# Kernel optimization log

Measured on AMD Instinct MI355X. Metric: run time of the kernel, lower is better.

Reference implementation:

```python
import jax, jax.numpy as jnp
import numpy as np

B = 2048          # number of graphs in the batch
ACT_DIM = 14      # nodes per graph (act_dim)
C = 128           # in_channels
H = 256           # hidden_size


def _pair_edges(n):
    ii, jj = np.meshgrid(np.arange(n), np.arange(n), indexing='ij')
    m = ii != jj
    return np.stack([ii[m], jj[m]], axis=1)  # [n*(n-1), 2]


def setup_inputs() -> dict:
    key = jax.random.key(0)
    ks = jax.random.split(key, 12)
    edges_np = _pair_edges(ACT_DIM)                       # [182, 2]
    offs = (np.arange(B) * ACT_DIM)[:, None, None]
    batched = (edges_np[None] + offs).reshape(-1, 2)      # [B*182, 2]
    edge_index = jnp.asarray(batched.T, dtype=jnp.int64 if jax.config.jax_enable_x64 else jnp.int32)
    edges = jnp.asarray(edges_np, dtype=jnp.int32)

    def lin(k, o, i):
        return jax.random.normal(k, (o, i), jnp.float32) * (1.0 / np.sqrt(i))

    return {
        'state': jax.random.normal(ks[0], (B * ACT_DIM, C), jnp.float32),
        'conv_w': lin(ks[1], C, C),
        'conv_b': jnp.zeros((C,), jnp.float32),
        'lin1_w': lin(ks[2], H, 2 * C),
        'lin1_b': jax.random.normal(ks[3], (H,), jnp.float32) * 0.01,
        'lin2_w': lin(ks[4], H, H),
        'lin2_b': jax.random.normal(ks[5], (H,), jnp.float32) * 0.01,
        'mu_w': lin(ks[6], 1, H),
        'mu_b': jnp.zeros((1,), jnp.float32),
        'sig_w': lin(ks[7], 1, H),
        'sig_b': jnp.zeros((1,), jnp.float32),
        'noise': jax.random.normal(ks[8], (B, edges_np.shape[0]), jnp.float32),
        'edge_index': edge_index,
        'edges': edges,
    }


def _gcn_conv(x, edge_index, w, b):
    # Standard GCNConv: add self-loops, symmetric normalization, x @ W^T, scatter-add, + bias.
    n = x.shape[0]
    loops = jnp.arange(n, dtype=edge_index.dtype)
    src = jnp.concatenate([edge_index[0], loops])
    dst = jnp.concatenate([edge_index[1], loops])
    deg = jax.ops.segment_sum(jnp.ones_like(src, dtype=x.dtype), dst, num_segments=n)
    dinv = jax.lax.rsqrt(deg)  # deg >= 1 because of self-loops
    norm = dinv[src] * dinv[dst]                       # [E+N]
    xw = x @ w.T                                       # [N, C]
    msg = xw[src] * norm[:, None]                      # gather + scale
    return jax.ops.segment_sum(msg, dst, num_segments=n) + b


def reference(state, conv_w, conv_b, lin1_w, lin1_b, lin2_w, lin2_b,
              mu_w, mu_b, sig_w, sig_b, noise, edge_index, edges):
    out = jax.nn.relu(_gcn_conv(state, edge_index, conv_w, conv_b))
    x = (out + state).reshape(-1, ACT_DIM, C)          # [B, 14, C]
    es, ed = edges[:, 0], edges[:, 1]
    ef = jnp.concatenate([x[:, es, :], x[:, ed, :]], axis=2)   # [B, E, 2C]
    h = jax.nn.leaky_relu(jnp.einsum('bec,hc->beh', ef, lin1_w) + lin1_b)
    h = jax.nn.leaky_relu(jnp.einsum('beh,gh->beg', h, lin2_w) + lin2_b)
    mu = jax.nn.softplus(jnp.einsum('beh,oh->beo', h, mu_w) + mu_b)[..., 0]   # [B, E]
    std = jax.nn.softplus(jnp.einsum('beh,oh->beo', h, sig_w) + sig_b)[..., 0]
    action = mu + std * noise                          # Normal rsample with fixed eps
    log_prob = jnp.sum(
        -0.5 * ((action - mu) / std) ** 2 - jnp.log(std) - 0.5 * jnp.log(2.0 * jnp.pi),
        axis=-1)                                       # [B]
    return action, log_prob
```

## Files before the change

kernel.cpp:

```cpp
#include <hip/hip_runtime.h>
#include <hip/hip_bf16.h>

#define ACT 14
#define CC 128
#define HH 256
#define EPB 182
#define NB 2048
#define M2 (NB*EPB)
#define NS 520
#define LP_CONST (-182.0f * 0.91893853320467274f)

typedef short s16x8 __attribute__((ext_vector_type(8)));
typedef float f32x4 __attribute__((ext_vector_type(4)));
typedef int   i32x4 __attribute__((ext_vector_type(4)));
typedef float f32x16 __attribute__((ext_vector_type(16)));

__device__ __forceinline__ short f2bf(float f) {
    unsigned u = __float_as_uint(f);
    unsigned r = (u + 0x7fffu + ((u >> 16) & 1u)) >> 16;
    return (short)r;
}
__device__ __forceinline__ float b2f(short s) {
    return __uint_as_float(((unsigned)(unsigned short)s) << 16);
}
__device__ __forceinline__ float bflo(int m) { return __uint_as_float(((unsigned)m) << 16); }
__device__ __forceinline__ float bfhi(int m) { return __uint_as_float((unsigned)m & 0xffff0000u); }
__device__ __forceinline__ float leaky(float x) { return fmaxf(x, 0.01f * x); }
__device__ __forceinline__ float softplusf(float x) { return x > 15.f ? x : log1pf(expf(x)); }

union bf2u { __hip_bfloat162 h; int i; };
__device__ __forceinline__ int pk_bf16(float a, float b) {
    bf2u u; u.h = __float22bfloat162_rn(make_float2(a, b));
    return u.i;
}

__global__ __launch_bounds__(256) void prep_kernel(
    const float* __restrict__ conv_w, const float* __restrict__ lin1_w,
    const float* __restrict__ lin2_w, const float* __restrict__ mu_w,
    const float* __restrict__ sig_w,
    short* __restrict__ W2bf, short* __restrict__ W1bf,
    short* __restrict__ cwTbf, short* __restrict__ w1sTbf,
    int* __restrict__ msbf)
{
    int i = blockIdx.x * 256 + threadIdx.x;
    W2bf[i] = f2bf(lin2_w[i]);
    {
        int n = i >> 7, k = i & 127;
        float v = (n < 256) ? lin1_w[n * 256 + k] : lin1_w[(n - 256) * 256 + 128 + k];
        W1bf[i] = f2bf(v);
    }
    if (i < 16384) {
        int k = i >> 7, j = i & 127;
        cwTbf[i] = f2bf(conv_w[j * 128 + k]);
    }
    if (i < 32768) {
        int k = i >> 8, h = i & 255;
        w1sTbf[i] = f2bf(lin1_w[h * 256 + k] + lin1_w[h * 256 + 128 + k]);
    }
    if (i < 256) msbf[i] = pk_bf16(mu_w[i], sig_w[i]);
}

__global__ __launch_bounds__(512, 4) void actor_kernel(
    const float* __restrict__ state, const short* __restrict__ W1bf,
    const short* __restrict__ W2bf,
    const short* __restrict__ cwTbf, const float* __restrict__ conv_b,
    const short* __restrict__ w1sTbf, const float* __restrict__ lin1_b,
    const float* __restrict__ lin2_b, const int* __restrict__ msbf,
    const float* __restrict__ mu_b, const float* __restrict__ sig_b,
    const float* __restrict__ noise, const int* __restrict__ edges,
    float* __restrict__ out)
{
    __shared__ short h1L[2][8192];
    __shared__ short nodeL[2 * ACT * NS];
    __shared__ float ssumL[2][128];
    __shared__ float gL[2][128];
    __shared__ float wL[2][256];
    __shared__ float b2L[256];
    __shared__ int   msL[256];
    __shared__ float mu_acc[384], sg_acc[384];
    __shared__ float lp_acc[2];

    short* stateL = &h1L[0][0];
    float* pp     = (float*)&h1L[0][5120];

    const int t = threadIdx.x, b = blockIdx.x;
    const int lane = t & 63, ln = lane & 15, q = lane >> 4;
    const int w = t >> 6;
    const int l32 = lane & 31, hf = lane >> 5;

    #pragma unroll
    for (int it = 0; it < 2; ++it) {
        int idx = it * 512 + t;
        int bt = idx >> 9, row = (idx >> 5) & 15, c4 = idx & 31;
        int kk = c4 >> 3, k8 = (c4 & 7) * 4;
        int* dst = (int*)&stateL[bt * 2560 + kk * 640 + row * 40 + k8];
        if (row < ACT) {
            f32x4 x = *(const f32x4*)(state + ((size_t)(2 * b + bt) * ACT + row) * CC + c4 * 4);
            dst[0] = pk_bf16(x[0], x[1]); dst[1] = pk_bf16(x[2], x[3]);
        } else { dst[0] = 0; dst[1] = 0; }
    }
    if (t < 256) {
        b2L[t] = lin2_b[t];
        msL[t] = msbf[t];
    } else {
        int i = t - 256, bt = i >> 7, c = i & 127;
        const float* sp = state + (size_t)(2 * b + bt) * ACT * CC + c;
        float s = 0.f;
        #pragma unroll
        for (int r = 0; r < ACT; ++r) s += sp[r * CC];
        ssumL[bt][c] = s * (1.f / 14.f);
    }
    if (t < 384) { mu_acc[t] = 0.f; sg_acc[t] = 0.f; }
    if (t < 2) lp_acc[t] = 0.f;
    __syncthreads();

    {
        int bt = t >> 8, s = (t >> 7) & 1, j = t & 127;
        const float* ss = ssumL[bt];
        float a0 = 0.f, a1 = 0.f;
        #pragma unroll 4
        for (int kk = 0; kk < 64; kk += 2) {
            int k = s * 64 + kk;
            a0 += b2f(cwTbf[k * 128 + j]) * ss[k];
            a1 += b2f(cwTbf[(k + 1) * 128 + j]) * ss[k + 1];
        }
        pp[t] = a0 + a1;
    }
    __syncthreads();
    if (t < 256) {
        int bt = t >> 7, j = t & 127;
        float a = pp[bt * 256 + j] + pp[bt * 256 + 128 + j] + conv_b[j];
        gL[bt][j] = fmaxf(a, 0.f);
    }
    __syncthreads();
    {
        int bt = t >> 8, h = t & 255;
        const float* gg = gL[bt];
        float a0 = 0.f, a1 = 0.f, a2 = 0.f, a3 = 0.f;
        #pragma unroll 2
        for (int k = 0; k < 128; k += 4) {
            a0 += b2f(w1sTbf[k * 256 + h]) * gg[k];
            a1 += b2f(w1sTbf[(k + 1) * 256 + h]) * gg[k + 1];
            a2 += b2f(w1sTbf[(k + 2) * 256 + h]) * gg[k + 2];
            a3 += b2f(w1sTbf[(k + 3) * 256 + h]) * gg[k + 3];
        }
        wL[bt][h] = (a0 + a1) + (a2 + a3) + lin1_b[h];
    }
    __syncthreads();

    f32x4 zero4 = {0.f, 0.f, 0.f, 0.f};
    f32x4 nacc[2][4];
    #pragma unroll
    for (int bt = 0; bt < 2; ++bt) {
        nacc[bt][0] = zero4; nacc[bt][1] = zero4;
        nacc[bt][2] = zero4; nacc[bt][3] = zero4;
    }
    #pragma unroll
    for (int c = 0; c < 4; ++c) {
        s16x8 a80 = *(const s16x8*)&stateL[0 * 2560 + c * 640 + ln * 40 + q * 8];
        s16x8 a81 = *(const s16x8*)&stateL[1 * 2560 + c * 640 + ln * 40 + q * 8];
        #pragma unroll
        for (int i = 0; i < 4; ++i) {
            int ct = w + 8 * i;
            s16x8 b8 = *(const s16x8*)&W1bf[(size_t)(ct * 16 + ln) * CC + c * 32 + q * 8];
            nacc[0][i] = __builtin_amdgcn_mfma_f32_16x16x32_bf16(a80, b8, nacc[0][i], 0, 0, 0);
            nacc[1][i] = __builtin_amdgcn_mfma_f32_16x16x32_bf16(a81, b8, nacc[1][i], 0, 0, 0);
        }
    }
    #pragma unroll
    for (int bt = 0; bt < 2; ++bt)
        #pragma unroll
        for (int i = 0; i < 4; ++i) {
            int col = (w + 8 * i) * 16 + ln;
            float wadd = (col < HH) ? wL[bt][col] : 0.f;
            #pragma unroll
            for (int rg = 0; rg < 4; ++rg) {
                int node = q * 4 + rg;
                if (node < ACT) nodeL[(bt * ACT + node) * NS + col] = f2bf(nacc[bt][i][rg] + wadd);
            }
        }

    s16x8 wa[16];
    #pragma unroll
    for (int c = 0; c < 16; ++c)
        wa[c] = *(const s16x8*)&W2bf[(size_t)(w * 32 + l32) * HH + c * 16 + hf * 8];
    __syncthreads();

    auto build = [&](int tile, int bufi) {
        int bt = (tile >= 6) ? 1 : 0;
        int e32 = t & 31;
        int e = (tile - bt * 6) * 32 + e32;
        bool ok = e < EPB;
        int base = bt * ACT * NS;
        int uo = base, vo = base + HH;
        if (ok) { int2 p = ((const int2*)edges)[e]; uo += p.x * NS; vo += p.y * NS; }
        int sl = t >> 5;
        #pragma unroll
        for (int s = 0; s < 2; ++s) {
            int slot = sl + 16 * s;
            int chunk = slot >> 1, half = slot & 1;
            int koff = chunk * 16 + half * 8;
            int o[4] = {0, 0, 0, 0};
            if (ok) {
                s16x8 u8 = *(const s16x8*)&nodeL[uo + koff];
                s16x8 v8 = *(const s16x8*)&nodeL[vo + koff];
                const int* ui = (const int*)&u8;
                const int* vi = (const int*)&v8;
                #pragma unroll
                for (int j = 0; j < 4; ++j) {
                    int uu = ui[j], vv = vi[j];
                    float s0 = bflo(uu) + bflo(vv);
                    float s1 = bfhi(uu) + bfhi(vv);
                    o[j] = pk_bf16(leaky(s0), leaky(s1));
                }
            }
            *(s16x8*)&h1L[bufi][chunk * 512 + (half * 32 + e32) * 8] = *(const s16x8*)o;
        }
    };

    build(0, 0);
    for (int tile = 0; tile < 12; ++tile) {
        __syncthreads();
        if (tile < 11) build(tile + 1, (tile + 1) & 1);
        const int buf = tile & 1;
        f32x16 acc;
        #pragma unroll
        for (int r = 0; r < 16; ++r) acc[r] = 0.f;
        #pragma unroll
        for (int c = 0; c < 16; ++c) {
            s16x8 b8 = *(const s16x8*)&h1L[buf][c * 512 + lane * 8];
            acc = __builtin_amdgcn_mfma_f32_32x32x16_bf16(wa[c], b8, acc, 0, 0, 0);
        }
        int bt = (tile >= 6) ? 1 : 0;
        int col0 = (tile - bt * 6) * 32;
        float pmu = 0.f, psg = 0.f;
        const int nsb = w * 32 + 4 * hf;
        #pragma unroll
        for (int g = 0; g < 4; ++g) {
            f32x4 b4 = *(const f32x4*)&b2L[nsb + 8 * g];
            i32x4 m4 = *(const i32x4*)&msL[nsb + 8 * g];
            #pragma unroll
            for (int i = 0; i < 4; ++i) {
                float h2 = leaky(acc[g * 4 + i] + b4[i]);
                pmu += bflo(m4[i]) * h2;
                psg += bfhi(m4[i]) * h2;
            }
        }
        pmu += __shfl_xor(pmu, 32);
        psg += __shfl_xor(psg, 32);
        if (lane < 32) {
            atomicAdd(&mu_acc[bt * 192 + col0 + l32], pmu);
            atomicAdd(&sg_acc[bt * 192 + col0 + l32], psg);
        }
    }
    __syncthreads();

    float lpv = 0.f;
    {
        int bt = t >> 8, i = t & 255;
        if (i < EPB) {
            float mu = softplusf(mu_acc[bt * 192 + i] + mu_b[0]);
            float sd = softplusf(sg_acc[bt * 192 + i] + sig_b[0]);
            float z = noise[(size_t)(2 * b + bt) * EPB + i];
            out[(size_t)(2 * b + bt) * EPB + i] = mu + sd * z;
            lpv = -0.5f * z * z - logf(sd);
        }
    }
    #pragma unroll
    for (int off = 1; off < 64; off <<= 1) lpv += __shfl_xor(lpv, off);
    if (lane == 0) atomicAdd(&lp_acc[t >> 8], lpv);
    __syncthreads();
    if (t < 2) out[M2 + 2 * b + t] = lp_acc[t] + LP_CONST;
}

extern "C" void kernel_launch(void* const* d_in, const int* in_sizes, int n_in,
                              void* d_out, int out_size, void* d_ws, size_t ws_size,
                              hipStream_t stream)
{
    const float* state  = (const float*)d_in[0];
    const float* conv_w = (const float*)d_in[1];
    const float* conv_b = (const float*)d_in[2];
    const float* lin1_w = (const float*)d_in[3];
    const float* lin1_b = (const float*)d_in[4];
    const float* lin2_w = (const float*)d_in[5];
    const float* lin2_b = (const float*)d_in[6];
    const float* mu_w   = (const float*)d_in[7];
    const float* mu_b   = (const float*)d_in[8];
    const float* sig_w  = (const float*)d_in[9];
    const float* sig_b  = (const float*)d_in[10];
    const float* noise  = (const float*)d_in[11];
    const int*   edges  = (const int*)d_in[13];
    float* out = (float*)d_out;

    char* ws = (char*)d_ws;
    short* W2bf   = (short*)ws;  ws += 65536 * 2;
    short* W1bf   = (short*)ws;  ws += 65536 * 2;
    short* cwTbf  = (short*)ws;  ws += 16384 * 2;
    short* w1sTbf = (short*)ws;  ws += 32768 * 2;
    int*   msbf   = (int*)ws;    ws += 256 * 4;

    prep_kernel<<<256, 256, 0, stream>>>(conv_w, lin1_w, lin2_w, mu_w, sig_w,
                                         W2bf, W1bf, cwTbf, w1sTbf, msbf);
    actor_kernel<<<NB / 2, 512, 0, stream>>>(state, W1bf, W2bf,
                                             cwTbf, conv_b, w1sTbf, lin1_b,
                                             lin2_b, msbf, mu_b, sig_b,
                                             noise, edges, out);
}
```

Baseline: 212.7 us.

## Process one graph per block instead of two and shrink shared memory

Each workgroup now handles a single graph, so the grid doubles to 2048 blocks and the per-block loops, accumulators and node buffers are halved. The scratch arrays for the conv and lin1 bias pre-pass are aliased into the h1 double buffer, and those reductions are split across more threads with an extra LDS combine step. This lowers LDS per block so more blocks can be resident and balances work across CUs. In exchange, each W1/W2 weight fragment loaded from global memory (including the 16-chunk W2 register preload) now serves one graph instead of two, so per-graph weight traffic and fixed setup cost double.

```diff
diff --git a/kernel.cpp b/kernel.cpp
--- a/kernel.cpp
+++ b/kernel.cpp
@@ -71,114 +71,103 @@
     float* __restrict__ out)
 {
     __shared__ short h1L[2][8192];
-    __shared__ short nodeL[2 * ACT * NS];
-    __shared__ float ssumL[2][128];
-    __shared__ float gL[2][128];
-    __shared__ float wL[2][256];
+    __shared__ short nodeL[ACT * NS];
     __shared__ float b2L[256];
     __shared__ int   msL[256];
-    __shared__ float mu_acc[384], sg_acc[384];
-    __shared__ float lp_acc[2];
+    __shared__ float mu_acc[192], sg_acc[192];
+    __shared__ float lp_acc[1];
 
     short* stateL = &h1L[0][0];
-    float* pp     = (float*)&h1L[0][5120];
+    float* pp     = (float*)&h1L[0][2560];
+    float* ssumL  = (float*)&h1L[0][3584];
+    float* gL     = (float*)&h1L[0][3840];
+    float* wL     = (float*)&h1L[0][4096];
 
     const int t = threadIdx.x, b = blockIdx.x;
     const int lane = t & 63, ln = lane & 15, q = lane >> 4;
     const int w = t >> 6;
     const int l32 = lane & 31, hf = lane >> 5;
 
-    #pragma unroll
-    for (int it = 0; it < 2; ++it) {
-        int idx = it * 512 + t;
-        int bt = idx >> 9, row = (idx >> 5) & 15, c4 = idx & 31;
+    {
+        int row = t >> 5, c4 = t & 31;
         int kk = c4 >> 3, k8 = (c4 & 7) * 4;
-        int* dst = (int*)&stateL[bt * 2560 + kk * 640 + row * 40 + k8];
+        int* dst = (int*)&stateL[kk * 640 + row * 40 + k8];
         if (row < ACT) {
-            f32x4 x = *(const f32x4*)(state + ((size_t)(2 * b + bt) * ACT + row) * CC + c4 * 4);
+            f32x4 x = *(const f32x4*)(state + ((size_t)b * ACT + row) * CC + c4 * 4);
             dst[0] = pk_bf16(x[0], x[1]); dst[1] = pk_bf16(x[2], x[3]);
         } else { dst[0] = 0; dst[1] = 0; }
     }
     if (t < 256) {
         b2L[t] = lin2_b[t];
         msL[t] = msbf[t];
-    } else {
-        int i = t - 256, bt = i >> 7, c = i & 127;
-        const float* sp = state + (size_t)(2 * b + bt) * ACT * CC + c;
+    } else if (t < 384) {
+        int c = t - 256;
+        const float* sp = state + (size_t)b * ACT * CC + c;
         float s = 0.f;
         #pragma unroll
         for (int r = 0; r < ACT; ++r) s += sp[r * CC];
-        ssumL[bt][c] = s * (1.f / 14.f);
-    }
-    if (t < 384) { mu_acc[t] = 0.f; sg_acc[t] = 0.f; }
-    if (t < 2) lp_acc[t] = 0.f;
-    __syncthreads();
-
-    {
-        int bt = t >> 8, s = (t >> 7) & 1, j = t & 127;
-        const float* ss = ssumL[bt];
+        ssumL[c] = s * (1.f / 14.f);
+    }
+    if (t < 192) { mu_acc[t] = 0.f; sg_acc[t] = 0.f; }
+    if (t == 0) lp_acc[0] = 0.f;
+    __syncthreads();
+
+    {
+        int s = t >> 7, j = t & 127;
         float a0 = 0.f, a1 = 0.f;
         #pragma unroll 4
-        for (int kk = 0; kk < 64; kk += 2) {
-            int k = s * 64 + kk;
-            a0 += b2f(cwTbf[k * 128 + j]) * ss[k];
-            a1 += b2f(cwTbf[(k + 1) * 128 + j]) * ss[k + 1];
+        for (int kk = 0; kk < 32; kk += 2) {
+            int k = s * 32 + kk;
+            a0 += b2f(cwTbf[k * 128 + j]) * ssumL[k];
+            a1 += b2f(cwTbf[(k + 1) * 128 + j]) * ssumL[k + 1];
         }
         pp[t] = a0 + a1;
     }
     __syncthreads();
-    if (t < 256) {
-        int bt = t >> 7, j = t & 127;
-        float a = pp[bt * 256 + j] + pp[bt * 256 + 128 + j] + conv_b[j];
-        gL[bt][j] = fmaxf(a, 0.f);
-    }
-    __syncthreads();
-    {
-        int bt = t >> 8, h = t & 255;
-        const float* gg = gL[bt];
+    if (t < 128) {
+        float a = pp[t] + pp[128 + t] + pp[256 + t] + pp[384 + t] + conv_b[t];
+        gL[t] = fmaxf(a, 0.f);
+    }
+    __syncthreads();
+    {
+        int s = t >> 8, h = t & 255;
         float a0 = 0.f, a1 = 0.f, a2 = 0.f, a3 = 0.f;
         #pragma unroll 2
-        for (int k = 0; k < 128; k += 4) {
-            a0 += b2f(w1sTbf[k * 256 + h]) * gg[k];
-            a1 += b2f(w1sTbf[(k + 1) * 256 + h]) * gg[k + 1];
-            a2 += b2f(w1sTbf[(k + 2) * 256 + h]) * gg[k + 2];
-            a3 += b2f(w1sTbf[(k + 3) * 256 + h]) * gg[k + 3];
-        }
-        wL[bt][h] = (a0 + a1) + (a2 + a3) + lin1_b[h];
-    }
+        for (int kk = 0; kk < 64; kk += 4) {
+            int k = s * 64 + kk;
+            a0 += b2f(w1sTbf[k * 256 + h]) * gL[k];
+            a1 += b2f(w1sTbf[(k + 1) * 256 + h]) * gL[k + 1];
+            a2 += b2f(w1sTbf[(k + 2) * 256 + h]) * gL[k + 2];
+            a3 += b2f(w1sTbf[(k + 3) * 256 + h]) * gL[k + 3];
+        }
+        pp[t] = (a0 + a1) + (a2 + a3);
+    }
+    __syncthreads();
+    if (t < 256) wL[t] = pp[t] + pp[256 + t] + lin1_b[t];
     __syncthreads();
 
     f32x4 zero4 = {0.f, 0.f, 0.f, 0.f};
-    f32x4 nacc[2][4];
-    #pragma unroll
-    for (int bt = 0; bt < 2; ++bt) {
-        nacc[bt][0] = zero4; nacc[bt][1] = zero4;
-        nacc[bt][2] = zero4; nacc[bt][3] = zero4;
-    }
+    f32x4 nacc[4] = {zero4, zero4, zero4, zero4};
     #pragma unroll
     for (int c = 0; c < 4; ++c) {
-        s16x8 a80 = *(const s16x8*)&stateL[0 * 2560 + c * 640 + ln * 40 + q * 8];
-        s16x8 a81 = *(const s16x8*)&stateL[1 * 2560 + c * 640 + ln * 40 + q * 8];
+        s16x8 a8 = *(const s16x8*)&stateL[c * 640 + ln * 40 + q * 8];
         #pragma unroll
         for (int i = 0; i < 4; ++i) {
             int ct = w + 8 * i;
             s16x8 b8 = *(const s16x8*)&W1bf[(size_t)(ct * 16 + ln) * CC + c * 32 + q * 8];
-            nacc[0][i] = __builtin_amdgcn_mfma_f32_16x16x32_bf16(a80, b8, nacc[0][i], 0, 0, 0);
-            nacc[1][i] = __builtin_amdgcn_mfma_f32_16x16x32_bf16(a81, b8, nacc[1][i], 0, 0, 0);
-        }
-    }
-    #pragma unroll
-    for (int bt = 0; bt < 2; ++bt)
-        #pragma unroll
-        for (int i = 0; i < 4; ++i) {
-            int col = (w + 8 * i) * 16 + ln;
-            float wadd = (col < HH) ? wL[bt][col] : 0.f;
-            #pragma unroll
-            for (int rg = 0; rg < 4; ++rg) {
-                int node = q * 4 + rg;
-                if (node < ACT) nodeL[(bt * ACT + node) * NS + col] = f2bf(nacc[bt][i][rg] + wadd);
-            }
-        }
+            nacc[i] = __builtin_amdgcn_mfma_f32_16x16x32_bf16(a8, b8, nacc[i], 0, 0, 0);
+        }
+    }
+    #pragma unroll
+    for (int i = 0; i < 4; ++i) {
+        int col = (w + 8 * i) * 16 + ln;
+        float wadd = (col < HH) ? wL[col] : 0.f;
+        #pragma unroll
+        for (int rg = 0; rg < 4; ++rg) {
+            int node = q * 4 + rg;
+            if (node < ACT) nodeL[node * NS + col] = f2bf(nacc[i][rg] + wadd);
+        }
+    }
 
     s16x8 wa[16];
     #pragma unroll
@@ -187,12 +176,10 @@
     __syncthreads();
 
     auto build = [&](int tile, int bufi) {
-        int bt = (tile >= 6) ? 1 : 0;
         int e32 = t & 31;
-        int e = (tile - bt * 6) * 32 + e32;
+        int e = tile * 32 + e32;
         bool ok = e < EPB;
-        int base = bt * ACT * NS;
-        int uo = base, vo = base + HH;
+        int uo = 0, vo = HH;
         if (ok) { int2 p = ((const int2*)edges)[e]; uo += p.x * NS; vo += p.y * NS; }
         int sl = t >> 5;
         #pragma unroll
@@ -219,9 +206,9 @@
     };
 
     build(0, 0);
-    for (int tile = 0; tile < 12; ++tile) {
+    for (int tile = 0; tile < 6; ++tile) {
         __syncthreads();
-        if (tile < 11) build(tile + 1, (tile + 1) & 1);
+        if (tile < 5) build(tile + 1, (tile + 1) & 1);
         const int buf = tile & 1;
         f32x16 acc;
         #pragma unroll
@@ -231,8 +218,7 @@
             s16x8 b8 = *(const s16x8*)&h1L[buf][c * 512 + lane * 8];
             acc = __builtin_amdgcn_mfma_f32_32x32x16_bf16(wa[c], b8, acc, 0, 0, 0);
         }
-        int bt = (tile >= 6) ? 1 : 0;
-        int col0 = (tile - bt * 6) * 32;
+        int col0 = tile * 32;
         float pmu = 0.f, psg = 0.f;
         const int nsb = w * 32 + 4 * hf;
         #pragma unroll
@@ -249,28 +235,25 @@
         pmu += __shfl_xor(pmu, 32);
         psg += __shfl_xor(psg, 32);
         if (lane < 32) {
-            atomicAdd(&mu_acc[bt * 192 + col0 + l32], pmu);
-            atomicAdd(&sg_acc[bt * 192 + col0 + l32], psg);
+            atomicAdd(&mu_acc[col0 + l32], pmu);
+            atomicAdd(&sg_acc[col0 + l32], psg);
         }
     }
     __syncthreads();
 
     float lpv = 0.f;
-    {
-        int bt = t >> 8, i = t & 255;
-        if (i < EPB) {
-            float mu = softplusf(mu_acc[bt * 192 + i] + mu_b[0]);
-            float sd = softplusf(sg_acc[bt * 192 + i] + sig_b[0]);
-            float z = noise[(size_t)(2 * b + bt) * EPB + i];
-            out[(size_t)(2 * b + bt) * EPB + i] = mu + sd * z;
-            lpv = -0.5f * z * z - logf(sd);
-        }
+    if (t < EPB) {
+        float mu = softplusf(mu_acc[t] + mu_b[0]);
+        float sd = softplusf(sg_acc[t] + sig_b[0]);
+        float z = noise[(size_t)b * EPB + t];
+        out[(size_t)b * EPB + t] = mu + sd * z;
+        lpv = -0.5f * z * z - logf(sd);
     }
     #pragma unroll
     for (int off = 1; off < 64; off <<= 1) lpv += __shfl_xor(lpv, off);
-    if (lane == 0) atomicAdd(&lp_acc[t >> 8], lpv);
-    __syncthreads();
-    if (t < 2) out[M2 + 2 * b + t] = lp_acc[t] + LP_CONST;
+    if (lane == 0) atomicAdd(&lp_acc[0], lpv);
+    __syncthreads();
+    if (t == 0) out[M2 + b] = lp_acc[0] + LP_CONST;
 }
 
 extern "C" void kernel_launch(void* const* d_in, const int* in_sizes, int n_in,
@@ -301,8 +284,8 @@
 
     prep_kernel<<<256, 256, 0, stream>>>(conv_w, lin1_w, lin2_w, mu_w, sig_w,
                                          W2bf, W1bf, cwTbf, w1sTbf, msbf);
-    actor_kernel<<<NB / 2, 512, 0, stream>>>(state, W1bf, W2bf,
-                                             cwTbf, conv_b, w1sTbf, lin1_b,
-                                             lin2_b, msbf, mu_b, sig_b,
-                                             noise, edges, out);
-}
+    actor_kernel<<<NB, 512, 0, stream>>>(state, W1bf, W2bf,
+                                         cwTbf, conv_b, w1sTbf, lin1_b,
+                                         lin2_b, msbf, mu_b, sig_b,
+                                         noise, edges, out);
+}
```

Measured after the change: 226.0 us. 1.06x slower.
